# Kernel optimization log

Measured on AMD Instinct MI355X. Metric: run time of the kernel, lower is better.

The kernel has to match this reference:

```python
import jax, jax.numpy as jnp
import numpy as np

BN_EPS = 1e-5
CLUSTER_SIZE = 32  # K (real clusters kept after softmax)


def setup_inputs() -> dict:
    key = jax.random.key(0)
    ks = jax.random.split(key, 7)
    B, N, D, Ktot, K = 4096, 128, 512, 48, 32
    x = jax.random.normal(ks[0], (B, N, D), dtype=jnp.float32)
    clusters = jax.random.normal(ks[1], (D, Ktot), dtype=jnp.float32) / np.sqrt(D)
    bn_w = jax.random.uniform(ks[2], (Ktot,), dtype=jnp.float32)
    bn_b = jax.random.normal(ks[3], (Ktot,), dtype=jnp.float32)
    bn_rm = jax.random.normal(ks[4], (Ktot,), dtype=jnp.float32)
    bn_rv = jax.random.uniform(ks[5], (Ktot,), dtype=jnp.float32)  # positive variance
    clusters2 = jax.random.normal(ks[6], (1, D, K), dtype=jnp.float32) / np.sqrt(D)
    return {"x": x, "clusters": clusters, "bn_w": bn_w, "bn_b": bn_b,
            "bn_rm": bn_rm, "bn_rv": bn_rv, "clusters2": clusters2}


def reference(x, clusters, bn_w, bn_b, bn_rm, bn_rv, clusters2):
    # x: [B, N, D]; clusters: [D, Ktot]; clusters2: [1, D, K]
    B, N, D = x.shape
    K = clusters2.shape[-1]
    # cluster projection: [B, N, Ktot]
    logits = jnp.einsum('bnd,dk->bnk', x, clusters)
    # inference BatchNorm1d (affine with running stats)
    inv_std = jax.lax.rsqrt(bn_rv + BN_EPS)
    logits = (logits - bn_rm) * inv_std * bn_w + bn_b
    # softmax over real + ghost clusters, then drop ghost (no renorm)
    assignment = jax.nn.softmax(logits, axis=-1)[..., :K]  # [B, N, K]
    a_sum = jnp.sum(assignment, axis=1, keepdims=True)      # [B, 1, K]
    a = a_sum * clusters2                                   # [B, D, K]
    # weighted VLAD accumulate: [B, D, K]
    vlad = jnp.einsum('bnk,bnd->bdk', assignment, x) - a
    # intra-normalize (L2 across descriptor dim D, per cluster)
    vlad = vlad / jnp.maximum(jnp.linalg.norm(vlad, axis=1, keepdims=True), 1e-12)
    # flatten and L2-normalize full vector
    vlad = vlad.reshape(B, D * K)
    vlad = vlad / jnp.maximum(jnp.linalg.norm(vlad, axis=1, keepdims=True), 1e-12)
    return vlad
```

## Files before the change

kernel.cpp:

```cpp
#include <hip/hip_runtime.h>

typedef unsigned short u16;
typedef unsigned int u32;
typedef __attribute__((ext_vector_type(8))) short short8;
typedef __attribute__((ext_vector_type(4))) float f32x4;
typedef __attribute__((ext_vector_type(4))) u32 u32x4;

#define NPT 128
#define DIM 512
#define KT 48
#define KC 32
#define BPB 16

__device__ __forceinline__ u16 f2bf(float f) {
    unsigned u = __builtin_bit_cast(unsigned, f);
    return (u16)((u + 0x7FFFu + ((u >> 16) & 1u)) >> 16);
}

__device__ __forceinline__ u32 cvtpk(float lo, float hi) {
    u32 r;
    asm("v_cvt_pk_bf16_f32 %0, %1, %2" : "=v"(r) : "v"(lo), "v"(hi));
    return r;
}

__device__ __forceinline__ void lds_barrier() {
    asm volatile("s_waitcnt lgkmcnt(0)" ::: "memory");
    __builtin_amdgcn_s_barrier();
}

__device__ __forceinline__ int swz(int n) {
    return ((n & 7) ^ ((n >> 3) & 7)) << 4;
}

__global__ void prep_kernel(const float* __restrict__ clusters,
                            const float* __restrict__ bn_w,
                            const float* __restrict__ bn_b,
                            const float* __restrict__ bn_rm,
                            const float* __restrict__ bn_rv,
                            u16* __restrict__ cTs,
                            float* __restrict__ tvec) {
    const int k = blockIdx.x;
    const float s = bn_w[k] * rsqrtf(bn_rv[k] + 1e-5f);
    if (threadIdx.x == 0) tvec[k] = bn_b[k] - bn_rm[k] * s;
    for (int d = threadIdx.x; d < DIM; d += blockDim.x)
        cTs[k * DIM + d] = f2bf(clusters[d * KT + k] * s);
}

__global__ __launch_bounds__(512)
void vlad_kernel(const float* __restrict__ x,
                 const float* __restrict__ c2,
                 const u16* __restrict__ cTs,
                 const float* __restrict__ tvec,
                 float* __restrict__ out) {
    __shared__ __align__(16) u16 cTsL[KT * DIM];
    __shared__ __align__(16) u16 buf[2][16 * DIM];
    __shared__ __align__(16) u16 aT[KC][136];
    __shared__ float asum_part[8][KC];
    __shared__ float colsq_part[8][KC];

    const int tid  = threadIdx.x;
    const int wave = tid >> 6;
    const int lane = tid & 63;
    const int lr   = lane & 15;
    const int lg   = lane >> 4;

    const int b0i = blockIdx.x * BPB;
    const float* xblk = x + (size_t)b0i * (NPT * DIM);

    const float t0 = tvec[lr], t1 = tvec[16 + lr], t2 = tvec[32 + lr];

    const int srow = tid >> 5;
    const int scol = (tid & 31) * 16;
    const int sbyte = scol * 2;
    const int ssw = swz(srow);

    #pragma unroll
    for (int i = 0; i < 6; ++i) {
        int idx = tid + i * 512;
        int k = idx >> 6, slot = idx & 63;
        u32x4 v = *(const u32x4*)(cTs + k * DIM + slot * 8);
        *(u32x4*)((char*)cTsL + k * 1024 + ((slot * 16) ^ swz(k))) = v;
    }
    {
        const float* g = xblk + srow * DIM + scol;
        f32x4 a0 = *(const f32x4*)(g);
        f32x4 a1 = *(const f32x4*)(g + 4);
        f32x4 a2 = *(const f32x4*)(g + 8);
        f32x4 a3 = *(const f32x4*)(g + 12);
        u32x4 wA, wB;
        wA[0] = cvtpk(a0[0], a0[1]); wA[1] = cvtpk(a0[2], a0[3]);
        wA[2] = cvtpk(a1[0], a1[1]); wA[3] = cvtpk(a1[2], a1[3]);
        wB[0] = cvtpk(a2[0], a2[1]); wB[1] = cvtpk(a2[2], a2[3]);
        wB[2] = cvtpk(a3[0], a3[1]); wB[3] = cvtpk(a3[2], a3[3]);
        char* dst = (char*)buf[0] + srow * 1024;
        *(u32x4*)(dst + (sbyte ^ ssw)) = wA;
        *(u32x4*)(dst + ((sbyte + 16) ^ ssw)) = wB;
    }
    __syncthreads();

    for (int m = 0; m < BPB; ++m) {
        f32x4 acc0 = {0.f,0.f,0.f,0.f}, acc1 = {0.f,0.f,0.f,0.f}, acc2 = {0.f,0.f,0.f,0.f};
        short8 af2[4][4];

        #pragma unroll
        for (int ns = 0; ns < 4; ++ns) {
            #pragma unroll
            for (int h = 0; h < 2; ++h) {
                const int j = ns * 2 + h;
                const int cur = j & 1;
                const int gnext = m * 8 + j + 1;
                const bool pOK = (gnext < BPB * 8);

                f32x4 a0, a1, a2, a3;
                if (pOK) {
                    const float* g = xblk + (size_t)gnext * (16 * DIM) + srow * DIM + scol;
                    a0 = *(const f32x4*)(g);
                    a1 = *(const f32x4*)(g + 4);
                    a2 = *(const f32x4*)(g + 8);
                    a3 = *(const f32x4*)(g + 12);
                }

                if ((lane >> 5) == h) {
                    const int nb = (lg & 1) * 8;
                    #pragma unroll
                    for (int dti = 0; dti < 4; ++dti) {
                        const int dd = wave * 128 + dti * 32 + 2 * lr;
                        short8 v;
                        #pragma unroll
                        for (int jj = 0; jj < 8; ++jj) {
                            const int rr = nb + jj;
                            v[jj] = *(const short*)((const char*)buf[cur] + rr * 1024 + (dd ^ swz(rr)));
                        }
                        af2[ns][dti] = v;
                    }
                }

                if (wave == j) {
                    const char* xb = (const char*)buf[cur] + lr * 1024;
                    const int sw = swz(lr);
                    const char* c0 = (const char*)cTsL + lr * 1024;
                    const char* c1 = (const char*)cTsL + (16 + lr) * 1024;
                    const char* c2p = (const char*)cTsL + (32 + lr) * 1024;
                    const int s1 = swz(16 + lr), s2 = swz(32 + lr);
                    #pragma unroll 2
                    for (int step = 0; step < 16; ++step) {
                        const int off = step * 64 + lg * 16;
                        short8 af  = *(const short8*)(xb + (off ^ sw));
                        short8 bb0 = *(const short8*)(c0 + (off ^ sw));
                        short8 bb1 = *(const short8*)(c1 + (off ^ s1));
                        short8 bb2 = *(const short8*)(c2p + (off ^ s2));
                        acc0 = __builtin_amdgcn_mfma_f32_16x16x32_bf16(af, bb0, acc0, 0, 0, 0);
                        acc1 = __builtin_amdgcn_mfma_f32_16x16x32_bf16(af, bb1, acc1, 0, 0, 0);
                        acc2 = __builtin_amdgcn_mfma_f32_16x16x32_bf16(af, bb2, acc2, 0, 0, 0);
                    }
                }

                if (pOK) {
                    u32x4 wA, wB;
                    wA[0] = cvtpk(a0[0], a0[1]); wA[1] = cvtpk(a0[2], a0[3]);
                    wA[2] = cvtpk(a1[0], a1[1]); wA[3] = cvtpk(a1[2], a1[3]);
                    wB[0] = cvtpk(a2[0], a2[1]); wB[1] = cvtpk(a2[2], a2[3]);
                    wB[2] = cvtpk(a3[0], a3[1]); wB[3] = cvtpk(a3[2], a3[3]);
                    char* dst = (char*)buf[cur ^ 1] + srow * 1024;
                    *(u32x4*)(dst + (sbyte ^ ssw)) = wA;
                    *(u32x4*)(dst + ((sbyte + 16) ^ ssw)) = wB;
                }
                lds_barrier();
            }
        }

        {
            float a0[4], a1[4];
            #pragma unroll
            for (int r = 0; r < 4; ++r) {
                float l0 = acc0[r] + t0, l1 = acc1[r] + t1, l2 = acc2[r] + t2;
                float mx = fmaxf(fmaxf(l0, l1), l2);
                #pragma unroll
                for (int o = 1; o < 16; o <<= 1) mx = fmaxf(mx, __shfl_xor(mx, o));
                float e0 = __expf(l0 - mx), e1 = __expf(l1 - mx), e2 = __expf(l2 - mx);
                float s = e0 + e1 + e2;
                #pragma unroll
                for (int o = 1; o < 16; o <<= 1) s += __shfl_xor(s, o);
                float inv = 1.0f / s;
                a0[r] = e0 * inv; a1[r] = e1 * inv;
            }
            float p0 = 0.f, p1 = 0.f;
            #pragma unroll
            for (int r = 0; r < 4; ++r) {
                int n = wave * 16 + lg * 4 + r;
                aT[lr][n]      = f2bf(a0[r]);
                aT[16 + lr][n] = f2bf(a1[r]);
                p0 += a0[r]; p1 += a1[r];
            }
            p0 += __shfl_xor(p0, 16); p0 += __shfl_xor(p0, 32);
            p1 += __shfl_xor(p1, 16); p1 += __shfl_xor(p1, 32);
            if (lane < 16) { asum_part[wave][lane] = p0; asum_part[wave][16 + lane] = p1; }
        }
        lds_barrier();

        f32x4 vacc[4][2];
        #pragma unroll
        for (int i = 0; i < 4; ++i) {
            vacc[i][0] = (f32x4){0.f,0.f,0.f,0.f};
            vacc[i][1] = (f32x4){0.f,0.f,0.f,0.f};
        }
        #pragma unroll
        for (int ns = 0; ns < 4; ++ns) {
            short8 bf0 = *(const short8*)(&aT[lr][ns * 32 + lg * 8]);
            short8 bf1 = *(const short8*)(&aT[16 + lr][ns * 32 + lg * 8]);
            #pragma unroll
            for (int dti = 0; dti < 4; ++dti) {
                vacc[dti][0] = __builtin_amdgcn_mfma_f32_16x16x32_bf16(af2[ns][dti], bf0, vacc[dti][0], 0, 0, 0);
                vacc[dti][1] = __builtin_amdgcn_mfma_f32_16x16x32_bf16(af2[ns][dti], bf1, vacc[dti][1], 0, 0, 0);
            }
        }

        float as0 = 0.f, as1 = 0.f;
        #pragma unroll
        for (int w2 = 0; w2 < 8; ++w2) {
            as0 += asum_part[w2][lr];
            as1 += asum_part[w2][16 + lr];
        }
        float cs0 = 0.f, cs1 = 0.f;
        #pragma unroll
        for (int dti = 0; dti < 4; ++dti) {
            #pragma unroll
            for (int r = 0; r < 4; ++r) {
                int d = (wave * 4 + dti) * 16 + lg * 4 + r;
                float v0 = vacc[dti][0][r] - as0 * c2[d * KC + lr];
                float v1 = vacc[dti][1][r] - as1 * c2[d * KC + 16 + lr];
                vacc[dti][0][r] = v0; vacc[dti][1][r] = v1;
                cs0 += v0 * v0; cs1 += v1 * v1;
            }
        }
        cs0 += __shfl_xor(cs0, 16); cs0 += __shfl_xor(cs0, 32);
        cs1 += __shfl_xor(cs1, 16); cs1 += __shfl_xor(cs1, 32);
        if (lane < 16) { colsq_part[wave][lane] = cs0; colsq_part[wave][16 + lane] = cs1; }
        lds_barrier();
        float sq0 = 0.f, sq1 = 0.f;
        #pragma unroll
        for (int w2 = 0; w2 < 8; ++w2) {
            sq0 += colsq_part[w2][lr];
            sq1 += colsq_part[w2][16 + lr];
        }
        float cn0 = sqrtf(sq0), cn1 = sqrtf(sq1);
        float s10 = 1.0f / fmaxf(cn0, 1e-12f);
        float s11 = 1.0f / fmaxf(cn1, 1e-12f);
        float c10 = cn0 * s10, c11 = cn1 * s11;
        float tot = c10 * c10 + c11 * c11;
        #pragma unroll
        for (int o = 1; o < 16; o <<= 1) tot += __shfl_xor(tot, o);
        float gs = 1.0f / fmaxf(sqrtf(tot), 1e-12f);
        float sk0 = s10 * gs, sk1 = s11 * gs;
        {
            float* ob = out + (size_t)(b0i + m) * (DIM * KC);
            #pragma unroll
            for (int dti = 0; dti < 4; ++dti) {
                #pragma unroll
                for (int r = 0; r < 4; ++r) {
                    int d = (wave * 4 + dti) * 16 + lg * 4 + r;
                    ob[d * KC + lr]      = vacc[dti][0][r] * sk0;
                    ob[d * KC + 16 + lr] = vacc[dti][1][r] * sk1;
                }
            }
        }
    }
}

extern "C" void kernel_launch(void* const* d_in, const int* in_sizes, int n_in,
                              void* d_out, int out_size, void* d_ws, size_t ws_size,
                              hipStream_t stream) {
    const float* x        = (const float*)d_in[0];
    const float* clusters = (const float*)d_in[1];
    const float* bn_w     = (const float*)d_in[2];
    const float* bn_b     = (const float*)d_in[3];
    const float* bn_rm    = (const float*)d_in[4];
    const float* bn_rv    = (const float*)d_in[5];
    const float* c2       = (const float*)d_in[6];
    float* out = (float*)d_out;

    u16*   cTs  = (u16*)d_ws;
    float* tvec = (float*)((char*)d_ws + KT * DIM * sizeof(u16));

    const int B = in_sizes[0] / (NPT * DIM);

    prep_kernel<<<KT, 256, 0, stream>>>(clusters, bn_w, bn_b, bn_rm, bn_rv, cTs, tvec);
    vlad_kernel<<<B / BPB, 512, 0, stream>>>(x, c2, cTs, tvec, out);
}
```

Measured before the change: 368.3 us.

## Deepen global prefetch to two chunks ahead with nontemporal loads and cache c2 in registers

The x-chunk prefetch now issues loads two chunks ahead into a two-slot register ring, so each load has a full iteration of MFMA work to hide behind before it is converted and written to LDS. Global x loads use nontemporal hints, since the data is streamed once. The per-batch c2 values are loaded into registers once per block rather than re-read from global memory for every batch item. This raises register pressure (32 extra floats for c2 plus another prefetch slot), which could lower occupancy.

```diff
diff --git a/kernel.cpp b/kernel.cpp
--- a/kernel.cpp
+++ b/kernel.cpp
@@ -11,6 +11,7 @@
 #define KT 48
 #define KC 32
 #define BPB 16
+#define NCH (BPB * 8)
 
 __device__ __forceinline__ u16 f2bf(float f) {
     unsigned u = __builtin_bit_cast(unsigned, f);
@@ -69,6 +70,14 @@
 
     const float t0 = tvec[lr], t1 = tvec[16 + lr], t2 = tvec[32 + lr];
 
+    float c2r0[16], c2r1[16];
+    #pragma unroll
+    for (int i = 0; i < 16; ++i) {
+        int d = (wave * 4 + (i >> 2)) * 16 + lg * 4 + (i & 3);
+        c2r0[i] = c2[d * KC + lr];
+        c2r1[i] = c2[d * KC + 16 + lr];
+    }
+
     const int srow = tid >> 5;
     const int scol = (tid & 31) * 16;
     const int sbyte = scol * 2;
@@ -83,10 +92,10 @@
     }
     {
         const float* g = xblk + srow * DIM + scol;
-        f32x4 a0 = *(const f32x4*)(g);
-        f32x4 a1 = *(const f32x4*)(g + 4);
-        f32x4 a2 = *(const f32x4*)(g + 8);
-        f32x4 a3 = *(const f32x4*)(g + 12);
+        f32x4 a0 = __builtin_nontemporal_load((const f32x4*)(g));
+        f32x4 a1 = __builtin_nontemporal_load((const f32x4*)(g + 4));
+        f32x4 a2 = __builtin_nontemporal_load((const f32x4*)(g + 8));
+        f32x4 a3 = __builtin_nontemporal_load((const f32x4*)(g + 12));
         u32x4 wA, wB;
         wA[0] = cvtpk(a0[0], a0[1]); wA[1] = cvtpk(a0[2], a0[3]);
         wA[2] = cvtpk(a1[0], a1[1]); wA[3] = cvtpk(a1[2], a1[3]);
@@ -96,6 +105,14 @@
         *(u32x4*)(dst + (sbyte ^ ssw)) = wA;
         *(u32x4*)(dst + ((sbyte + 16) ^ ssw)) = wB;
     }
+    f32x4 z[2][4];
+    {
+        const float* g = xblk + (size_t)1 * (16 * DIM) + srow * DIM + scol;
+        z[1][0] = __builtin_nontemporal_load((const f32x4*)(g));
+        z[1][1] = __builtin_nontemporal_load((const f32x4*)(g + 4));
+        z[1][2] = __builtin_nontemporal_load((const f32x4*)(g + 8));
+        z[1][3] = __builtin_nontemporal_load((const f32x4*)(g + 12));
+    }
     __syncthreads();
 
     for (int m = 0; m < BPB; ++m) {
@@ -107,17 +124,14 @@
             #pragma unroll
             for (int h = 0; h < 2; ++h) {
                 const int j = ns * 2 + h;
-                const int cur = j & 1;
-                const int gnext = m * 8 + j + 1;
-                const bool pOK = (gnext < BPB * 8);
-
-                f32x4 a0, a1, a2, a3;
-                if (pOK) {
-                    const float* g = xblk + (size_t)gnext * (16 * DIM) + srow * DIM + scol;
-                    a0 = *(const f32x4*)(g);
-                    a1 = *(const f32x4*)(g + 4);
-                    a2 = *(const f32x4*)(g + 8);
-                    a3 = *(const f32x4*)(g + 12);
+                const int g = m * 8 + j;
+
+                if (g + 2 < NCH) {
+                    const float* gp = xblk + (size_t)(g + 2) * (16 * DIM) + srow * DIM + scol;
+                    z[h][0] = __builtin_nontemporal_load((const f32x4*)(gp));
+                    z[h][1] = __builtin_nontemporal_load((const f32x4*)(gp + 4));
+                    z[h][2] = __builtin_nontemporal_load((const f32x4*)(gp + 8));
+                    z[h][3] = __builtin_nontemporal_load((const f32x4*)(gp + 12));
                 }
 
                 if ((lane >> 5) == h) {
@@ -129,14 +143,14 @@
                         #pragma unroll
                         for (int jj = 0; jj < 8; ++jj) {
                             const int rr = nb + jj;
-                            v[jj] = *(const short*)((const char*)buf[cur] + rr * 1024 + (dd ^ swz(rr)));
+                            v[jj] = *(const short*)((const char*)buf[h] + rr * 1024 + (dd ^ swz(rr)));
                         }
                         af2[ns][dti] = v;
                     }
                 }
 
                 if (wave == j) {
-                    const char* xb = (const char*)buf[cur] + lr * 1024;
+                    const char* xb = (const char*)buf[h] + lr * 1024;
                     const int sw = swz(lr);
                     const char* c0 = (const char*)cTsL + lr * 1024;
                     const char* c1 = (const char*)cTsL + (16 + lr) * 1024;
@@ -155,13 +169,17 @@
                     }
                 }
 
-                if (pOK) {
+                if (g + 1 < NCH) {
                     u32x4 wA, wB;
-                    wA[0] = cvtpk(a0[0], a0[1]); wA[1] = cvtpk(a0[2], a0[3]);
-                    wA[2] = cvtpk(a1[0], a1[1]); wA[3] = cvtpk(a1[2], a1[3]);
-                    wB[0] = cvtpk(a2[0], a2[1]); wB[1] = cvtpk(a2[2], a2[3]);
-                    wB[2] = cvtpk(a3[0], a3[1]); wB[3] = cvtpk(a3[2], a3[3]);
-                    char* dst = (char*)buf[cur ^ 1] + srow * 1024;
+                    wA[0] = cvtpk(z[h ^ 1][0][0], z[h ^ 1][0][1]);
+                    wA[1] = cvtpk(z[h ^ 1][0][2], z[h ^ 1][0][3]);
+                    wA[2] = cvtpk(z[h ^ 1][1][0], z[h ^ 1][1][1]);
+                    wA[3] = cvtpk(z[h ^ 1][1][2], z[h ^ 1][1][3]);
+                    wB[0] = cvtpk(z[h ^ 1][2][0], z[h ^ 1][2][1]);
+                    wB[1] = cvtpk(z[h ^ 1][2][2], z[h ^ 1][2][3]);
+                    wB[2] = cvtpk(z[h ^ 1][3][0], z[h ^ 1][3][1]);
+                    wB[3] = cvtpk(z[h ^ 1][3][2], z[h ^ 1][3][3]);
+                    char* dst = (char*)buf[h ^ 1] + srow * 1024;
                     *(u32x4*)(dst + (sbyte ^ ssw)) = wA;
                     *(u32x4*)(dst + ((sbyte + 16) ^ ssw)) = wB;
                 }
@@ -226,9 +244,8 @@
         for (int dti = 0; dti < 4; ++dti) {
             #pragma unroll
             for (int r = 0; r < 4; ++r) {
-                int d = (wave * 4 + dti) * 16 + lg * 4 + r;
-                float v0 = vacc[dti][0][r] - as0 * c2[d * KC + lr];
-                float v1 = vacc[dti][1][r] - as1 * c2[d * KC + 16 + lr];
+                float v0 = vacc[dti][0][r] - as0 * c2r0[dti * 4 + r];
+                float v1 = vacc[dti][1][r] - as1 * c2r1[dti * 4 + r];
                 vacc[dti][0][r] = v0; vacc[dti][1][r] = v1;
                 cs0 += v0 * v0; cs1 += v1 * v1;
             }
```

Result: slower. 399.2 us (+8.4%).

## Prefetch next batch's first two x chunks across the softmax/VLAD epilogue

Applied to the files above, without the earlier changes.

Restructures the x-chunk double-buffer pipeline so each batch element's first two 16-row chunks are loaded before the epilogue and written to LDS during it. Within a batch, prefetch now only covers chunks 2..7, so the global-load latency for the next batch element overlaps the softmax and VLAD MFMA work instead of sitting on the in-loop critical path. It also raises wave priority around the logits MFMA loop. The cost is more live registers (eight f32x4) during the epilogue and LDS buffer writes that must not race with reads of buf in the epilogue.

```diff
diff --git a/kernel.cpp b/kernel.cpp
--- a/kernel.cpp
+++ b/kernel.cpp
@@ -81,8 +81,9 @@
         u32x4 v = *(const u32x4*)(cTs + k * DIM + slot * 8);
         *(u32x4*)((char*)cTsL + k * 1024 + ((slot * 16) ^ swz(k))) = v;
     }
-    {
-        const float* g = xblk + srow * DIM + scol;
+    #pragma unroll
+    for (int c = 0; c < 2; ++c) {
+        const float* g = xblk + (size_t)c * (16 * DIM) + srow * DIM + scol;
         f32x4 a0 = *(const f32x4*)(g);
         f32x4 a1 = *(const f32x4*)(g + 4);
         f32x4 a2 = *(const f32x4*)(g + 8);
@@ -92,7 +93,7 @@
         wA[2] = cvtpk(a1[0], a1[1]); wA[3] = cvtpk(a1[2], a1[3]);
         wB[0] = cvtpk(a2[0], a2[1]); wB[1] = cvtpk(a2[2], a2[3]);
         wB[2] = cvtpk(a3[0], a3[1]); wB[3] = cvtpk(a3[2], a3[3]);
-        char* dst = (char*)buf[0] + srow * 1024;
+        char* dst = (char*)buf[c] + srow * 1024;
         *(u32x4*)(dst + (sbyte ^ ssw)) = wA;
         *(u32x4*)(dst + ((sbyte + 16) ^ ssw)) = wB;
     }
@@ -107,13 +108,11 @@
             #pragma unroll
             for (int h = 0; h < 2; ++h) {
                 const int j = ns * 2 + h;
-                const int cur = j & 1;
-                const int gnext = m * 8 + j + 1;
-                const bool pOK = (gnext < BPB * 8);
+                const bool sOK = (j >= 1 && j <= 6);
 
                 f32x4 a0, a1, a2, a3;
-                if (pOK) {
-                    const float* g = xblk + (size_t)gnext * (16 * DIM) + srow * DIM + scol;
+                if (sOK) {
+                    const float* g = xblk + (size_t)(m * 8 + j + 1) * (16 * DIM) + srow * DIM + scol;
                     a0 = *(const f32x4*)(g);
                     a1 = *(const f32x4*)(g + 4);
                     a2 = *(const f32x4*)(g + 8);
@@ -129,14 +128,15 @@
                         #pragma unroll
                         for (int jj = 0; jj < 8; ++jj) {
                             const int rr = nb + jj;
-                            v[jj] = *(const short*)((const char*)buf[cur] + rr * 1024 + (dd ^ swz(rr)));
+                            v[jj] = *(const short*)((const char*)buf[h] + rr * 1024 + (dd ^ swz(rr)));
                         }
                         af2[ns][dti] = v;
                     }
                 }
 
                 if (wave == j) {
-                    const char* xb = (const char*)buf[cur] + lr * 1024;
+                    __builtin_amdgcn_s_setprio(1);
+                    const char* xb = (const char*)buf[h] + lr * 1024;
                     const int sw = swz(lr);
                     const char* c0 = (const char*)cTsL + lr * 1024;
                     const char* c1 = (const char*)cTsL + (16 + lr) * 1024;
@@ -153,20 +153,36 @@
                         acc1 = __builtin_amdgcn_mfma_f32_16x16x32_bf16(af, bb1, acc1, 0, 0, 0);
                         acc2 = __builtin_amdgcn_mfma_f32_16x16x32_bf16(af, bb2, acc2, 0, 0, 0);
                     }
-                }
-
-                if (pOK) {
+                    __builtin_amdgcn_s_setprio(0);
+                }
+
+                if (sOK) {
                     u32x4 wA, wB;
                     wA[0] = cvtpk(a0[0], a0[1]); wA[1] = cvtpk(a0[2], a0[3]);
                     wA[2] = cvtpk(a1[0], a1[1]); wA[3] = cvtpk(a1[2], a1[3]);
                     wB[0] = cvtpk(a2[0], a2[1]); wB[1] = cvtpk(a2[2], a2[3]);
                     wB[2] = cvtpk(a3[0], a3[1]); wB[3] = cvtpk(a3[2], a3[3]);
-                    char* dst = (char*)buf[cur ^ 1] + srow * 1024;
+                    char* dst = (char*)buf[h ^ 1] + srow * 1024;
                     *(u32x4*)(dst + (sbyte ^ ssw)) = wA;
                     *(u32x4*)(dst + ((sbyte + 16) ^ ssw)) = wB;
                 }
                 lds_barrier();
             }
+        }
+
+        const bool tOK = (m + 1 < BPB);
+        f32x4 zn[8];
+        if (tOK) {
+            const float* nb = xblk + (size_t)(m + 1) * (NPT * DIM) + srow * DIM + scol;
+            zn[0] = *(const f32x4*)(nb);
+            zn[1] = *(const f32x4*)(nb + 4);
+            zn[2] = *(const f32x4*)(nb + 8);
+            zn[3] = *(const f32x4*)(nb + 12);
+            const float* nb1 = nb + 16 * DIM;
+            zn[4] = *(const f32x4*)(nb1);
+            zn[5] = *(const f32x4*)(nb1 + 4);
+            zn[6] = *(const f32x4*)(nb1 + 8);
+            zn[7] = *(const f32x4*)(nb1 + 12);
         }
 
         {
@@ -215,6 +231,24 @@
             }
         }
 
+        if (tOK) {
+            u32x4 wA, wB;
+            wA[0] = cvtpk(zn[0][0], zn[0][1]); wA[1] = cvtpk(zn[0][2], zn[0][3]);
+            wA[2] = cvtpk(zn[1][0], zn[1][1]); wA[3] = cvtpk(zn[1][2], zn[1][3]);
+            wB[0] = cvtpk(zn[2][0], zn[2][1]); wB[1] = cvtpk(zn[2][2], zn[2][3]);
+            wB[2] = cvtpk(zn[3][0], zn[3][1]); wB[3] = cvtpk(zn[3][2], zn[3][3]);
+            char* dst0 = (char*)buf[0] + srow * 1024;
+            *(u32x4*)(dst0 + (sbyte ^ ssw)) = wA;
+            *(u32x4*)(dst0 + ((sbyte + 16) ^ ssw)) = wB;
+            wA[0] = cvtpk(zn[4][0], zn[4][1]); wA[1] = cvtpk(zn[4][2], zn[4][3]);
+            wA[2] = cvtpk(zn[5][0], zn[5][1]); wA[3] = cvtpk(zn[5][2], zn[5][3]);
+            wB[0] = cvtpk(zn[6][0], zn[6][1]); wB[1] = cvtpk(zn[6][2], zn[6][3]);
+            wB[2] = cvtpk(zn[7][0], zn[7][1]); wB[3] = cvtpk(zn[7][2], zn[7][3]);
+            char* dst1 = (char*)buf[1] + srow * 1024;
+            *(u32x4*)(dst1 + (sbyte ^ ssw)) = wA;
+            *(u32x4*)(dst1 + ((sbyte + 16) ^ ssw)) = wB;
+        }
+
         float as0 = 0.f, as1 = 0.f;
         #pragma unroll
         for (int w2 = 0; w2 < 8; ++w2) {
```

Measured after the change: 481.5 us. 1.31x slower.

## Split logits GEMM across all waves along D with LDS partial-sum reduction

Applied to the files above, without the earlier changes.

Previously, for each 16-row chunk of points, only one wave computed the full 512-deep logits GEMM while the other waves idled. Now every wave computes a 64-wide slice of D for each chunk, writes its partial logits to LDS, and a second barrier phase sums the eight partials into a logits buffer. The global prefetch is also moved one more chunk ahead through register staging. This spreads MFMA work evenly across waves, at the cost of an extra barrier per chunk, extra LDS traffic and more shared memory, which may lower occupancy.

```diff
diff --git a/kernel.cpp b/kernel.cpp
--- a/kernel.cpp
+++ b/kernel.cpp
@@ -11,6 +11,9 @@
 #define KT 48
 #define KC 32
 #define BPB 16
+#define NCH (BPB * 8)
+#define LPAD 52
+#define PBW (16 * LPAD + 4)
 
 __device__ __forceinline__ u16 f2bf(float f) {
     unsigned u = __builtin_bit_cast(unsigned, f);
@@ -55,6 +58,8 @@
     __shared__ __align__(16) u16 cTsL[KT * DIM];
     __shared__ __align__(16) u16 buf[2][16 * DIM];
     __shared__ __align__(16) u16 aT[KC][136];
+    __shared__ float pbuf[8 * PBW];
+    __shared__ float logitsL[NPT * LPAD];
     __shared__ float asum_part[8][KC];
     __shared__ float colsq_part[8][KC];
 
@@ -96,10 +101,17 @@
         *(u32x4*)(dst + (sbyte ^ ssw)) = wA;
         *(u32x4*)(dst + ((sbyte + 16) ^ ssw)) = wB;
     }
+    f32x4 z[4];
+    {
+        const float* g = xblk + (size_t)1 * (16 * DIM) + srow * DIM + scol;
+        z[0] = *(const f32x4*)(g);
+        z[1] = *(const f32x4*)(g + 4);
+        z[2] = *(const f32x4*)(g + 8);
+        z[3] = *(const f32x4*)(g + 12);
+    }
     __syncthreads();
 
     for (int m = 0; m < BPB; ++m) {
-        f32x4 acc0 = {0.f,0.f,0.f,0.f}, acc1 = {0.f,0.f,0.f,0.f}, acc2 = {0.f,0.f,0.f,0.f};
         short8 af2[4][4];
 
         #pragma unroll
@@ -107,17 +119,24 @@
             #pragma unroll
             for (int h = 0; h < 2; ++h) {
                 const int j = ns * 2 + h;
-                const int cur = j & 1;
-                const int gnext = m * 8 + j + 1;
-                const bool pOK = (gnext < BPB * 8);
-
-                f32x4 a0, a1, a2, a3;
-                if (pOK) {
-                    const float* g = xblk + (size_t)gnext * (16 * DIM) + srow * DIM + scol;
-                    a0 = *(const f32x4*)(g);
-                    a1 = *(const f32x4*)(g + 4);
-                    a2 = *(const f32x4*)(g + 8);
-                    a3 = *(const f32x4*)(g + 12);
+                const int g = m * 8 + j;
+
+                if (g + 1 < NCH) {
+                    u32x4 wA, wB;
+                    wA[0] = cvtpk(z[0][0], z[0][1]); wA[1] = cvtpk(z[0][2], z[0][3]);
+                    wA[2] = cvtpk(z[1][0], z[1][1]); wA[3] = cvtpk(z[1][2], z[1][3]);
+                    wB[0] = cvtpk(z[2][0], z[2][1]); wB[1] = cvtpk(z[2][2], z[2][3]);
+                    wB[2] = cvtpk(z[3][0], z[3][1]); wB[3] = cvtpk(z[3][2], z[3][3]);
+                    char* dst = (char*)buf[h ^ 1] + srow * 1024;
+                    *(u32x4*)(dst + (sbyte ^ ssw)) = wA;
+                    *(u32x4*)(dst + ((sbyte + 16) ^ ssw)) = wB;
+                }
+                if (g + 2 < NCH) {
+                    const float* gp = xblk + (size_t)(g + 2) * (16 * DIM) + srow * DIM + scol;
+                    z[0] = *(const f32x4*)(gp);
+                    z[1] = *(const f32x4*)(gp + 4);
+                    z[2] = *(const f32x4*)(gp + 8);
+                    z[3] = *(const f32x4*)(gp + 12);
                 }
 
                 if ((lane >> 5) == h) {
@@ -129,51 +148,69 @@
                         #pragma unroll
                         for (int jj = 0; jj < 8; ++jj) {
                             const int rr = nb + jj;
-                            v[jj] = *(const short*)((const char*)buf[cur] + rr * 1024 + (dd ^ swz(rr)));
+                            v[jj] = *(const short*)((const char*)buf[h] + rr * 1024 + (dd ^ swz(rr)));
                         }
                         af2[ns][dti] = v;
                     }
                 }
 
-                if (wave == j) {
-                    const char* xb = (const char*)buf[cur] + lr * 1024;
+                f32x4 p0 = {0.f,0.f,0.f,0.f}, p1 = {0.f,0.f,0.f,0.f}, p2 = {0.f,0.f,0.f,0.f};
+                {
                     const int sw = swz(lr);
-                    const char* c0 = (const char*)cTsL + lr * 1024;
-                    const char* c1 = (const char*)cTsL + (16 + lr) * 1024;
-                    const char* c2p = (const char*)cTsL + (32 + lr) * 1024;
+                    const char* xb  = (const char*)buf[h] + lr * 1024;
+                    const char* cb0 = (const char*)cTsL + lr * 1024;
+                    const char* cb1 = (const char*)cTsL + (16 + lr) * 1024;
+                    const char* cb2 = (const char*)cTsL + (32 + lr) * 1024;
                     const int s1 = swz(16 + lr), s2 = swz(32 + lr);
-                    #pragma unroll 2
-                    for (int step = 0; step < 16; ++step) {
-                        const int off = step * 64 + lg * 16;
-                        short8 af  = *(const short8*)(xb + (off ^ sw));
-                        short8 bb0 = *(const short8*)(c0 + (off ^ sw));
-                        short8 bb1 = *(const short8*)(c1 + (off ^ s1));
-                        short8 bb2 = *(const short8*)(c2p + (off ^ s2));
-                        acc0 = __builtin_amdgcn_mfma_f32_16x16x32_bf16(af, bb0, acc0, 0, 0, 0);
-                        acc1 = __builtin_amdgcn_mfma_f32_16x16x32_bf16(af, bb1, acc1, 0, 0, 0);
-                        acc2 = __builtin_amdgcn_mfma_f32_16x16x32_bf16(af, bb2, acc2, 0, 0, 0);
+                    #pragma unroll
+                    for (int ss = 0; ss < 2; ++ss) {
+                        const int off = (wave * 2 + ss) * 64 + lg * 16;
+                        short8 af = *(const short8*)(xb  + (off ^ sw));
+                        short8 b0 = *(const short8*)(cb0 + (off ^ sw));
+                        short8 b1 = *(const short8*)(cb1 + (off ^ s1));
+                        short8 b2 = *(const short8*)(cb2 + (off ^ s2));
+                        p0 = __builtin_amdgcn_mfma_f32_16x16x32_bf16(af, b0, p0, 0, 0, 0);
+                        p1 = __builtin_amdgcn_mfma_f32_16x16x32_bf16(af, b1, p1, 0, 0, 0);
+                        p2 = __builtin_amdgcn_mfma_f32_16x16x32_bf16(af, b2, p2, 0, 0, 0);
                     }
                 }
-
-                if (pOK) {
-                    u32x4 wA, wB;
-                    wA[0] = cvtpk(a0[0], a0[1]); wA[1] = cvtpk(a0[2], a0[3]);
-                    wA[2] = cvtpk(a1[0], a1[1]); wA[3] = cvtpk(a1[2], a1[3]);
-                    wB[0] = cvtpk(a2[0], a2[1]); wB[1] = cvtpk(a2[2], a2[3]);
-                    wB[2] = cvtpk(a3[0], a3[1]); wB[3] = cvtpk(a3[2], a3[3]);
-                    char* dst = (char*)buf[cur ^ 1] + srow * 1024;
-                    *(u32x4*)(dst + (sbyte ^ ssw)) = wA;
-                    *(u32x4*)(dst + ((sbyte + 16) ^ ssw)) = wB;
+                {
+                    float* pw = pbuf + wave * PBW;
+                    #pragma unroll
+                    for (int r = 0; r < 4; ++r) {
+                        int row = lg * 4 + r;
+                        pw[row * LPAD + lr]      = p0[r];
+                        pw[row * LPAD + 16 + lr] = p1[r];
+                        pw[row * LPAD + 32 + lr] = p2[r];
+                    }
                 }
                 lds_barrier();
+
+                #pragma unroll
+                for (int half = 0; half < 2; ++half) {
+                    int s = tid + half * 512;
+                    int k = s & 63, row = s >> 6;
+                    if (k < KT) {
+                        float acc = 0.f;
+                        #pragma unroll
+                        for (int w2 = 0; w2 < 8; ++w2)
+                            acc += pbuf[w2 * PBW + row * LPAD + k];
+                        logitsL[(j * 16 + row) * LPAD + k] = acc;
+                    }
+                }
+                lds_barrier();
             }
         }
 
         {
+            const float* lrow = logitsL + (wave * 16) * LPAD;
             float a0[4], a1[4];
             #pragma unroll
             for (int r = 0; r < 4; ++r) {
-                float l0 = acc0[r] + t0, l1 = acc1[r] + t1, l2 = acc2[r] + t2;
+                int row = lg * 4 + r;
+                float l0 = lrow[row * LPAD + lr]      + t0;
+                float l1 = lrow[row * LPAD + 16 + lr] + t1;
+                float l2 = lrow[row * LPAD + 32 + lr] + t2;
                 float mx = fmaxf(fmaxf(l0, l1), l2);
                 #pragma unroll
                 for (int o = 1; o < 16; o <<= 1) mx = fmaxf(mx, __shfl_xor(mx, o));
```

New measurement: 374.8 us. About the same (+1.8%).
